# Performance work log

Measured on AMD Instinct MI355X. Metric: run time of the kernel, lower is better.

## Reference

```python
import jax, jax.numpy as jnp
import numpy as np

B, D, F, FH = 8, 16, 16, 128
L = D * D
EPS = 1e-5


def _coords():
    i = np.arange(L, dtype=np.float64)
    c0 = ((i + 1) / D - D / 2) / (D / 2)
    c1 = ((i + 1) % D - D / 2) / (D / 2)
    return jnp.asarray(np.stack([c0, c1], axis=1), dtype=jnp.float32)  # (L, 2)


def setup_inputs() -> dict:
    key = jax.random.key(0)
    ks = jax.random.split(key, 16)
    s = 0.05
    fin = F + 2
    inp = {
        "x": jax.random.normal(ks[0], (B, F, D, D), jnp.float32),
        # g_fc1 weight split into the x_i half (first f+2 cols) and x_j half
        "W1a": jax.random.normal(ks[1], (fin, FH), jnp.float32) * s,
        "W1b": jax.random.normal(ks[2], (fin, FH), jnp.float32) * s,
        "b1": jnp.zeros((FH,), jnp.float32),
        "g1_gamma": jnp.ones((FH,), jnp.float32), "g1_beta": jnp.zeros((FH,), jnp.float32),
        "W2": jax.random.normal(ks[3], (FH, FH), jnp.float32) * s, "b2": jnp.zeros((FH,), jnp.float32),
        "g2_gamma": jnp.ones((FH,), jnp.float32), "g2_beta": jnp.zeros((FH,), jnp.float32),
        "W3": jax.random.normal(ks[4], (FH, FH), jnp.float32) * s, "b3": jnp.zeros((FH,), jnp.float32),
        "g3_gamma": jnp.ones((FH,), jnp.float32), "g3_beta": jnp.zeros((FH,), jnp.float32),
        "Wagg": jax.random.normal(ks[5], (L,), jnp.float32) * s, "bagg": jnp.zeros((), jnp.float32),
        "Wf": jax.random.normal(ks[6], (FH, FH), jnp.float32) * s, "bf": jnp.zeros((FH,), jnp.float32),
        "f_gamma": jnp.ones((FH,), jnp.float32), "f_beta": jnp.zeros((FH,), jnp.float32),
        "Wo2": jax.random.normal(ks[7], (FH, FH), jnp.float32) * s, "bo2": jnp.zeros((FH,), jnp.float32),
        "o2_gamma": jnp.ones((FH,), jnp.float32), "o2_beta": jnp.zeros((FH,), jnp.float32),
        "Wo3": jax.random.normal(ks[8], (FH, F), jnp.float32) * s, "bo3": jnp.zeros((F,), jnp.float32),
        "coord": _coords(),
    }
    return inp


def _bn(h, gamma, beta):
    # torch BatchNorm1d (training mode) applied over channel dim = last axis here;
    # stats over (batch, length), biased variance.
    mu = jnp.mean(h, axis=(0, 1))
    var = jnp.mean((h - mu) ** 2, axis=(0, 1))
    return gamma * (h - mu) * jax.lax.rsqrt(var + EPS) + beta


def reference(x, W1a, W1b, b1, g1_gamma, g1_beta, W2, b2, g2_gamma, g2_beta,
              W3, b3, g3_gamma, g3_beta, Wagg, bagg, Wf, bf, f_gamma, f_beta,
              Wo2, bo2, o2_gamma, o2_beta, Wo3, bo3, coord):
    b, f, d = x.shape[0], x.shape[1], x.shape[2]
    l = d * d
    x_flat = x.reshape(b, f, l).transpose(0, 2, 1)                     # (b, L, f)
    x_flat = jnp.concatenate([x_flat, jnp.broadcast_to(coord, (b, l, 2))], axis=2)  # (b, L, f+2)
    # g_fc1 on cat([x_i, x_j]): x_i varies along pair-dim2 (index l), x_j along dim1 (index k)
    hi = x_flat @ W1a                                                  # (b, L, FH)
    hj = x_flat @ W1b                                                  # (b, L, FH)
    h = hi[:, None, :, :] + hj[:, :, None, :] + b1                     # (b, L, L, FH)
    h = h.reshape(b, l * l, -1)
    h = jax.nn.relu(_bn(h, g1_gamma, g1_beta))
    h = jax.nn.relu(_bn(h @ W2 + b2, g2_gamma, g2_beta))
    h = jax.nn.relu(_bn(h @ W3 + b3, g3_gamma, g3_beta))
    x_g = h.reshape(b, l, l, -1)                                       # (b, k, l, FH)
    # affine_aggregate: Linear(L -> 1) over the l (dim2) axis after permute
    x_agg = jnp.einsum('bklf,l->bkf', x_g, Wagg) + bagg                # (b, L, FH)
    x_f = jax.nn.relu(_bn(x_agg @ Wf + bf, f_gamma, f_beta))
    xo = jax.nn.relu(_bn(x_f @ Wo2 + bo2, o2_gamma, o2_beta))
    out = xo @ Wo3 + bo3                                               # (b, L, f)
    return out.reshape(b, d, d, f).transpose(0, 3, 1, 2)               # (b, f, d, d)
```

## Files before the change

kernel.cpp:

```cpp
#include <hip/hip_runtime.h>
#include <hip/hip_bf16.h>

typedef __bf16 bf16x8 __attribute__((ext_vector_type(8)));
typedef float  f32x4  __attribute__((ext_vector_type(4)));

static constexpr size_t MB = 1u << 20;
static constexpr size_t HI_OFF  = 0;
static constexpr size_t HJ_OFF  = HI_OFF + MB;
static constexpr size_t Z_OFF   = HJ_OFF + MB;
static constexpr size_t PS_OFF  = Z_OFF + (size_t)524288 * 128 * 2;
static constexpr size_t PQ_OFF  = PS_OFF + (size_t)4096 * 128 * 4;
static constexpr size_t S1I_OFF = PQ_OFF + (size_t)4096 * 128 * 4;
static constexpr size_t S2I_OFF = S1I_OFF + 32768;
static constexpr size_t S1J_OFF = S2I_OFF + 32768;
static constexpr size_t S2J_OFF = S1J_OFF + 32768;
static constexpr size_t A1_OFF  = S2J_OFF + 32768;
static constexpr size_t D1_OFF  = A1_OFF + 512;
static constexpr size_t A2_OFF  = D1_OFF + 512;
static constexpr size_t C2_OFF  = A2_OFF + 512;
static constexpr size_t A3_OFF  = C2_OFF + 512;
static constexpr size_t C3_OFF  = A3_OFF + 512;
static constexpr size_t AF_OFF  = C3_OFF + 512;
static constexpr size_t CF_OFF  = AF_OFF + 512;
static constexpr size_t AO_OFF  = CF_OFF + 512;
static constexpr size_t CO_OFF  = AO_OFF + 512;
static constexpr size_t W2T_OFF = CO_OFF + 512;
static constexpr size_t W3T_OFF = W2T_OFF + 32768;
static constexpr size_t XAGG_OFF = W3T_OFF + 32768;
static constexpr size_t Y1_OFF  = XAGG_OFF + MB;
static constexpr size_t Y2_OFF  = Y1_OFF + MB;
static constexpr size_t TPS_OFF = Y2_OFF + MB;
static constexpr size_t TPQ_OFF = TPS_OFF + 65536;

__global__ void build_h(const float* __restrict__ x, const float* __restrict__ coord,
                        const float* __restrict__ W1a, const float* __restrict__ W1b,
                        float* __restrict__ hi, float* __restrict__ hj)
{
    __shared__ float xr[18];
    int bl = blockIdx.x;
    int b = bl >> 8, l = bl & 255;
    int t = threadIdx.x;
    if (t < 18)
        xr[t] = (t < 16) ? x[((size_t)b * 16 + t) * 256 + l] : coord[l * 2 + (t - 16)];
    __syncthreads();
    float ai = 0.f, aj = 0.f;
#pragma unroll
    for (int c = 0; c < 18; ++c) {
        float xv = xr[c];
        ai += xv * W1a[c * 128 + t];
        aj += xv * W1b[c * 128 + t];
    }
    hi[(size_t)bl * 128 + t] = ai;
    hj[(size_t)bl * 128 + t] = aj;
}

__global__ void stats1(const float* __restrict__ hi, const float* __restrict__ hj,
                       float* __restrict__ S1i, float* __restrict__ S2i,
                       float* __restrict__ S1j, float* __restrict__ S2j)
{
    int g = blockIdx.x;
    int b = g >> 3, lg = g & 7;
    int f = threadIdx.x;
    float s1i = 0, s2i = 0, s1j = 0, s2j = 0;
#pragma unroll 4
    for (int i = 0; i < 32; ++i) {
        int l = lg * 32 + i;
        float vi = hi[((size_t)b * 256 + l) * 128 + f];
        float vj = hj[((size_t)b * 256 + l) * 128 + f];
        s1i += vi; s2i += vi * vi;
        s1j += vj; s2j += vj * vj;
    }
    S1i[g * 128 + f] = s1i; S2i[g * 128 + f] = s2i;
    S1j[g * 128 + f] = s1j; S2j[g * 128 + f] = s2j;
}

__global__ void bn1_finalize(const float* __restrict__ S1i, const float* __restrict__ S2i,
                             const float* __restrict__ S1j, const float* __restrict__ S2j,
                             const float* __restrict__ g, const float* __restrict__ be,
                             float* __restrict__ a1, float* __restrict__ d1)
{
    int f = threadIdx.x;
    float s1i = 0, s2i = 0, s1j = 0, s2j = 0;
    float mib[8], mjb[8];
#pragma unroll
    for (int b = 0; b < 8; ++b) {
        float sb = 0, sbj = 0;
#pragma unroll
        for (int lg = 0; lg < 8; ++lg) {
            int gg = b * 8 + lg;
            sb  += S1i[gg * 128 + f]; s2i += S2i[gg * 128 + f];
            sbj += S1j[gg * 128 + f]; s2j += S2j[gg * 128 + f];
        }
        mib[b] = sb * (1.f / 256.f); mjb[b] = sbj * (1.f / 256.f);
        s1i += sb; s1j += sbj;
    }
    const float invN = 1.f / 2048.f;
    float mi = s1i * invN, mj = s1j * invN;
    float vu = s2i * invN - mi * mi;
    float vv = s2j * invN - mj * mj;
    float cr = 0.f;
#pragma unroll
    for (int b = 0; b < 8; ++b) cr += (mib[b] - mi) * (mjb[b] - mj);
    cr *= (1.f / 8.f);
    float var = vu + vv + 2.f * cr;
    float av = g[f] * rsqrtf(var + 1e-5f);
    a1[f] = av;
    d1[f] = be[f] - av * (mi + mj);
}

__global__ void transpose_w(const float* __restrict__ W2, const float* __restrict__ W3,
                            __bf16* __restrict__ W2t, __bf16* __restrict__ W3t)
{
    int f = blockIdx.x, k = threadIdx.x;
    W2t[f * 128 + k] = (__bf16)W2[k * 128 + f];
    W3t[f * 128 + k] = (__bf16)W3[k * 128 + f];
}

__global__ __launch_bounds__(256, 3) void pair_gemm1(
    const float* __restrict__ hi, const float* __restrict__ hj,
    const float* __restrict__ a1, const float* __restrict__ d1,
    const __bf16* __restrict__ W2t,
    __bf16* __restrict__ Z, float* __restrict__ ps, float* __restrict__ pq)
{
    __shared__ __align__(16) char hA[32768];

    int blk = blockIdx.x;
    int half = blk & 1;
    int bk = blk >> 1;
    int b = bk >> 8;
    int t = threadIdx.x;
    int lane = t & 63;
    int wave = t >> 6;
    int fc = (t & 15) * 8;
    int rg = t >> 4;
    int cl = lane & 15;
    int kg = lane >> 4;
    int colbase = wave * 32;

    bf16x8 Bf[2][4];
#pragma unroll
    for (int n = 0; n < 2; ++n) {
        const __bf16* wp = W2t + (colbase + n * 16 + cl) * 128 + kg * 8;
#pragma unroll
        for (int kk = 0; kk < 4; ++kk)
            Bf[n][kk] = *reinterpret_cast<const bf16x8*>(wp + kk * 32);
    }

    float a1v[8], qv[8];
    const float* hjrow = hj + (size_t)bk * 128 + fc;
    const float* d1p = d1 + fc;
    const float* a1p = a1 + fc;
#pragma unroll
    for (int j = 0; j < 8; ++j) { a1v[j] = a1p[j]; qv[j] = a1v[j] * hjrow[j] + d1p[j]; }

    const float* hib = hi + ((size_t)b * 256 + half * 128) * 128;
#pragma unroll
    for (int rr = 0; rr < 128; rr += 16) {
        int row = rr + rg;
        const float* src = hib + row * 128 + fc;
        bf16x8 v;
#pragma unroll
        for (int j = 0; j < 8; ++j) {
            float h = fmaxf(a1v[j] * src[j] + qv[j], 0.f);
            v[j] = (__bf16)h;
        }
        int byte = (row * 256 + fc * 2) ^ ((row & 7) << 4);
        *reinterpret_cast<bf16x8*>(hA + byte) = v;
    }
    __syncthreads();

    f32x4 acc[8][2] = {};
#pragma unroll
    for (int kk = 0; kk < 128; kk += 32) {
        bf16x8 af[8];
#pragma unroll
        for (int m = 0; m < 8; ++m) {
            int row = m * 16 + cl;
            int byte = (row * 256 + (kk + kg * 8) * 2) ^ ((row & 7) << 4);
            af[m] = *reinterpret_cast<const bf16x8*>(hA + byte);
        }
#pragma unroll
        for (int m = 0; m < 8; ++m)
#pragma unroll
            for (int n = 0; n < 2; ++n)
                acc[m][n] = __builtin_amdgcn_mfma_f32_16x16x32_bf16(af[m], Bf[n][kk >> 5], acc[m][n], 0, 0, 0);
    }

    __bf16* zb = Z + ((size_t)bk * 256 + half * 128) * 128;
    int r0 = kg * 4;
#pragma unroll
    for (int n = 0; n < 2; ++n) {
        float s = 0.f, q = 0.f;
#pragma unroll
        for (int m = 0; m < 8; ++m)
#pragma unroll
            for (int r = 0; r < 4; ++r) {
                float v = acc[m][n][r];
                zb[(m * 16 + r0 + r) * 128 + colbase + n * 16 + cl] = (__bf16)v;
                s += v; q += v * v;
            }
        s += __shfl_xor(s, 16); s += __shfl_xor(s, 32);
        q += __shfl_xor(q, 16); q += __shfl_xor(q, 32);
        if (lane < 16) {
            ps[(size_t)blk * 128 + colbase + n * 16 + cl] = s;
            pq[(size_t)blk * 128 + colbase + n * 16 + cl] = q;
        }
    }
}

__global__ __launch_bounds__(256, 3) void pair_gemm2(
    __bf16* __restrict__ Z,
    const float* __restrict__ a2, const float* __restrict__ c2,
    const __bf16* __restrict__ W3t,
    float* __restrict__ ps, float* __restrict__ pq)
{
    __shared__ __align__(16) char hA[32768];

    int blk = blockIdx.x;
    int half = blk & 1;
    int bk = blk >> 1;
    int t = threadIdx.x;
    int lane = t & 63;
    int wave = t >> 6;
    int fc = (t & 15) * 8;
    int rg = t >> 4;
    int cl = lane & 15;
    int kg = lane >> 4;
    int colbase = wave * 32;

    bf16x8 Bf[2][4];
#pragma unroll
    for (int n = 0; n < 2; ++n) {
        const __bf16* wp = W3t + (colbase + n * 16 + cl) * 128 + kg * 8;
#pragma unroll
        for (int kk = 0; kk < 4; ++kk)
            Bf[n][kk] = *reinterpret_cast<const bf16x8*>(wp + kk * 32);
    }

    float a2v[8], c2v[8];
#pragma unroll
    for (int j = 0; j < 8; ++j) { a2v[j] = a2[fc + j]; c2v[j] = c2[fc + j]; }

    __bf16* zbase = Z + ((size_t)bk * 256 + half * 128) * 128;
#pragma unroll
    for (int rr = 0; rr < 128; rr += 16) {
        int row = rr + rg;
        bf16x8 zv = *reinterpret_cast<const bf16x8*>(zbase + row * 128 + fc);
        bf16x8 v;
#pragma unroll
        for (int j = 0; j < 8; ++j) {
            float h = fmaxf(a2v[j] * (float)zv[j] + c2v[j], 0.f);
            v[j] = (__bf16)h;
        }
        int byte = (row * 256 + fc * 2) ^ ((row & 7) << 4);
        *reinterpret_cast<bf16x8*>(hA + byte) = v;
    }
    __syncthreads();

    f32x4 acc[8][2] = {};
#pragma unroll
    for (int kk = 0; kk < 128; kk += 32) {
        bf16x8 af[8];
#pragma unroll
        for (int m = 0; m < 8; ++m) {
            int row = m * 16 + cl;
            int byte = (row * 256 + (kk + kg * 8) * 2) ^ ((row & 7) << 4);
            af[m] = *reinterpret_cast<const bf16x8*>(hA + byte);
        }
#pragma unroll
        for (int m = 0; m < 8; ++m)
#pragma unroll
            for (int n = 0; n < 2; ++n)
                acc[m][n] = __builtin_amdgcn_mfma_f32_16x16x32_bf16(af[m], Bf[n][kk >> 5], acc[m][n], 0, 0, 0);
    }

    int r0 = kg * 4;
#pragma unroll
    for (int n = 0; n < 2; ++n) {
        float s = 0.f, q = 0.f;
#pragma unroll
        for (int m = 0; m < 8; ++m)
#pragma unroll
            for (int r = 0; r < 4; ++r) {
                float v = acc[m][n][r];
                zbase[(m * 16 + r0 + r) * 128 + colbase + n * 16 + cl] = (__bf16)v;
                s += v; q += v * v;
            }
        s += __shfl_xor(s, 16); s += __shfl_xor(s, 32);
        q += __shfl_xor(q, 16); q += __shfl_xor(q, 32);
        if (lane < 16) {
            ps[(size_t)blk * 128 + colbase + n * 16 + cl] = s;
            pq[(size_t)blk * 128 + colbase + n * 16 + cl] = q;
        }
    }
}

__global__ void finalize_bn(const float* __restrict__ ps, const float* __restrict__ pq,
                            int nblk, float inv_count,
                            const float* __restrict__ gamma, const float* __restrict__ beta,
                            float* __restrict__ a, float* __restrict__ c)
{
    __shared__ float rs[256], rq[256];
    int f = blockIdx.x, t = threadIdx.x;
    float s = 0, q = 0;
    for (int i = t; i < nblk; i += 256) {
        s += ps[(size_t)i * 128 + f];
        q += pq[(size_t)i * 128 + f];
    }
    rs[t] = s; rq[t] = q;
    __syncthreads();
    for (int st = 128; st > 0; st >>= 1) {
        if (t < st) { rs[t] += rs[t + st]; rq[t] += rq[t + st]; }
        __syncthreads();
    }
    if (t == 0) {
        float mean = rs[0] * inv_count;
        float var = rq[0] * inv_count - mean * mean;
        float av = gamma[f] * rsqrtf(var + 1e-5f);
        a[f] = av;
        c[f] = beta[f] - av * mean;
    }
}

__global__ __launch_bounds__(256) void aggregate(
    const __bf16* __restrict__ Z,
    const float* __restrict__ a3, const float* __restrict__ c3,
    const float* __restrict__ Wagg, const float* __restrict__ bagg,
    float* __restrict__ xagg)
{
    __shared__ float red[16 * 128];
    int bk = blockIdx.x;
    int t = threadIdx.x;
    int fc = t & 15;
    int g = t >> 4;
    float av[8], cv[8];
#pragma unroll
    for (int j = 0; j < 8; ++j) { av[j] = a3[fc * 8 + j]; cv[j] = c3[fc * 8 + j]; }

    const __bf16* zb = Z + (size_t)bk * 256 * 128;
    float acc[8] = {};
#pragma unroll 4
    for (int i = 0; i < 16; ++i) {
        int l = g * 16 + i;
        bf16x8 zv = *reinterpret_cast<const bf16x8*>(zb + (size_t)l * 128 + fc * 8);
        float w = Wagg[l];
#pragma unroll
        for (int j = 0; j < 8; ++j)
            acc[j] += fmaxf(av[j] * (float)zv[j] + cv[j], 0.f) * w;
    }
#pragma unroll
    for (int j = 0; j < 8; ++j) red[g * 128 + fc * 8 + j] = acc[j];
    __syncthreads();
    if (t < 128) {
        float s = 0;
#pragma unroll
        for (int gg = 0; gg < 16; ++gg) s += red[gg * 128 + t];
        xagg[(size_t)bk * 128 + t] = s + bagg[0];
    }
}

__global__ void tail_gemm(const float* __restrict__ X,
                          const float* __restrict__ aIn, const float* __restrict__ cIn, int relu_in,
                          const float* __restrict__ W, const float* __restrict__ bias,
                          float* __restrict__ Y, float* __restrict__ ps, float* __restrict__ pq)
{
    __shared__ float xs[2048];
    __shared__ float rsum[256];
    int blk = blockIdx.x, t = threadIdx.x;
    for (int i = t; i < 2048; i += 256) {
        float v = X[(size_t)blk * 2048 + i];
        if (relu_in) { int f = i & 127; v = fmaxf(aIn[f] * v + cIn[f], 0.f); }
        xs[i] = v;
    }
    __syncthreads();
    int col = t & 127, hf = t >> 7;
    float bv = bias[col];
    float acc[8];
#pragma unroll
    for (int r = 0; r < 8; ++r) acc[r] = bv;
    for (int k = 0; k < 128; ++k) {
        float w = W[k * 128 + col];
#pragma unroll
        for (int r = 0; r < 8; ++r) acc[r] += xs[(hf * 8 + r) * 128 + k] * w;
    }
    float s = 0, q = 0;
#pragma unroll
    for (int r = 0; r < 8; ++r) {
        Y[((size_t)blk * 16 + hf * 8 + r) * 128 + col] = acc[r];
        s += acc[r]; q += acc[r] * acc[r];
    }
    rsum[t] = s; __syncthreads();
    if (hf == 0) ps[(size_t)blk * 128 + col] = rsum[col] + rsum[128 + col];
    __syncthreads();
    rsum[t] = q; __syncthreads();
    if (hf == 0) pq[(size_t)blk * 128 + col] = rsum[col] + rsum[128 + col];
}

__global__ void tail_out(const float* __restrict__ Y2,
                         const float* __restrict__ ao, const float* __restrict__ co,
                         const float* __restrict__ Wo3, const float* __restrict__ bo3,
                         float* __restrict__ out)
{
    __shared__ float xs[2048];
    int blk = blockIdx.x, t = threadIdx.x;
    for (int i = t; i < 2048; i += 256) {
        int f = i & 127;
        xs[i] = fmaxf(ao[f] * Y2[(size_t)blk * 2048 + i] + co[f], 0.f);
    }
    __syncthreads();
    int col = t & 15, r = t >> 4;
    float acc = bo3[col];
    for (int k = 0; k < 128; ++k) acc += xs[r * 128 + k] * Wo3[k * 16 + col];
    int grow = blk * 16 + r;
    int b = grow >> 8, l = grow & 255;
    out[((size_t)b * 16 + col) * 256 + l] = acc;
}

extern "C" void kernel_launch(void* const* d_in, const int* in_sizes, int n_in,
                              void* d_out, int out_size, void* d_ws, size_t ws_size,
                              hipStream_t stream)
{
    const float* x     = (const float*)d_in[0];
    const float* W1a   = (const float*)d_in[1];
    const float* W1b   = (const float*)d_in[2];
    const float* g1g   = (const float*)d_in[4];
    const float* g1b   = (const float*)d_in[5];
    const float* W2    = (const float*)d_in[6];
    const float* g2g   = (const float*)d_in[8];
    const float* g2b   = (const float*)d_in[9];
    const float* W3    = (const float*)d_in[10];
    const float* g3g   = (const float*)d_in[12];
    const float* g3b   = (const float*)d_in[13];
    const float* Wagg  = (const float*)d_in[14];
    const float* bagg  = (const float*)d_in[15];
    const float* Wf    = (const float*)d_in[16];
    const float* bf_   = (const float*)d_in[17];
    const float* fg    = (const float*)d_in[18];
    const float* fb    = (const float*)d_in[19];
    const float* Wo2   = (const float*)d_in[20];
    const float* bo2   = (const float*)d_in[21];
    const float* og    = (const float*)d_in[22];
    const float* ob    = (const float*)d_in[23];
    const float* Wo3   = (const float*)d_in[24];
    const float* bo3   = (const float*)d_in[25];
    const float* coord = (const float*)d_in[26];

    char* ws = (char*)d_ws;
    float*  HI   = (float*)(ws + HI_OFF);
    float*  HJ   = (float*)(ws + HJ_OFF);
    __bf16* Z    = (__bf16*)(ws + Z_OFF);
    float*  PS   = (float*)(ws + PS_OFF);
    float*  PQ   = (float*)(ws + PQ_OFF);
    float*  S1I  = (float*)(ws + S1I_OFF);
    float*  S2I  = (float*)(ws + S2I_OFF);
    float*  S1J  = (float*)(ws + S1J_OFF);
    float*  S2J  = (float*)(ws + S2J_OFF);
    float*  A1   = (float*)(ws + A1_OFF);
    float*  D1   = (float*)(ws + D1_OFF);
    float*  A2   = (float*)(ws + A2_OFF);
    float*  C2   = (float*)(ws + C2_OFF);
    float*  A3   = (float*)(ws + A3_OFF);
    float*  C3   = (float*)(ws + C3_OFF);
    float*  AF   = (float*)(ws + AF_OFF);
    float*  CF   = (float*)(ws + CF_OFF);
    float*  AO   = (float*)(ws + AO_OFF);
    float*  CO   = (float*)(ws + CO_OFF);
    __bf16* W2T  = (__bf16*)(ws + W2T_OFF);
    __bf16* W3T  = (__bf16*)(ws + W3T_OFF);
    float*  XAGG = (float*)(ws + XAGG_OFF);
    float*  Y1   = (float*)(ws + Y1_OFF);
    float*  Y2   = (float*)(ws + Y2_OFF);
    float*  TPS  = (float*)(ws + TPS_OFF);
    float*  TPQ  = (float*)(ws + TPQ_OFF);

    build_h<<<2048, 128, 0, stream>>>(x, coord, W1a, W1b, HI, HJ);
    stats1<<<64, 128, 0, stream>>>(HI, HJ, S1I, S2I, S1J, S2J);
    bn1_finalize<<<1, 128, 0, stream>>>(S1I, S2I, S1J, S2J, g1g, g1b, A1, D1);
    transpose_w<<<128, 128, 0, stream>>>(W2, W3, W2T, W3T);

    pair_gemm1<<<4096, 256, 0, stream>>>(HI, HJ, A1, D1, W2T, Z, PS, PQ);
    finalize_bn<<<128, 256, 0, stream>>>(PS, PQ, 4096, 1.f / 524288.f, g2g, g2b, A2, C2);

    pair_gemm2<<<4096, 256, 0, stream>>>(Z, A2, C2, W3T, PS, PQ);
    finalize_bn<<<128, 256, 0, stream>>>(PS, PQ, 4096, 1.f / 524288.f, g3g, g3b, A3, C3);

    aggregate<<<2048, 256, 0, stream>>>(Z, A3, C3, Wagg, bagg, XAGG);

    tail_gemm<<<128, 256, 0, stream>>>(XAGG, A1, D1, 0, Wf, bf_, Y1, TPS, TPQ);
    finalize_bn<<<128, 256, 0, stream>>>(TPS, TPQ, 128, 1.f / 2048.f, fg, fb, AF, CF);

    tail_gemm<<<128, 256, 0, stream>>>(Y1, AF, CF, 1, Wo2, bo2, Y2, TPS, TPQ);
    finalize_bn<<<128, 256, 0, stream>>>(TPS, TPQ, 128, 1.f / 2048.f, og, ob, AO, CO);

    tail_out<<<128, 256, 0, stream>>>(Y2, AO, CO, Wo3, bo3, (float*)d_out);

    (void)in_sizes; (void)n_in; (void)out_size; (void)ws_size;
}
```

Baseline: 197.9 us.

## Fuse tail BN finalize into consumer kernels and raise pair GEMM occupancy

Removes the two small finalize_bn launches in the tail MLP. Each consumer block now reduces the partial sums itself and applies the BN affine plus ReLU. Separate stats buffers are added so that consumer kernels do not read buffers still being overwritten. The pair GEMMs get launch_bounds raised from 3 to 4 blocks per SM, and their epilogue is reordered to sweep rows with both column tiles per row, which may improve store coalescing. The fused finalize repeats the reduction in every block, and the higher occupancy target may cause register spills with 64 accumulator floats per thread.

```diff
diff --git a/kernel.cpp b/kernel.cpp
--- a/kernel.cpp
+++ b/kernel.cpp
@@ -20,17 +20,15 @@
 static constexpr size_t C2_OFF  = A2_OFF + 512;
 static constexpr size_t A3_OFF  = C2_OFF + 512;
 static constexpr size_t C3_OFF  = A3_OFF + 512;
-static constexpr size_t AF_OFF  = C3_OFF + 512;
-static constexpr size_t CF_OFF  = AF_OFF + 512;
-static constexpr size_t AO_OFF  = CF_OFF + 512;
-static constexpr size_t CO_OFF  = AO_OFF + 512;
-static constexpr size_t W2T_OFF = CO_OFF + 512;
+static constexpr size_t W2T_OFF = C3_OFF + 512;
 static constexpr size_t W3T_OFF = W2T_OFF + 32768;
 static constexpr size_t XAGG_OFF = W3T_OFF + 32768;
 static constexpr size_t Y1_OFF  = XAGG_OFF + MB;
 static constexpr size_t Y2_OFF  = Y1_OFF + MB;
 static constexpr size_t TPS_OFF = Y2_OFF + MB;
 static constexpr size_t TPQ_OFF = TPS_OFF + 65536;
+static constexpr size_t TPS2_OFF = TPQ_OFF + 65536;
+static constexpr size_t TPQ2_OFF = TPS2_OFF + 65536;
 
 __global__ void build_h(const float* __restrict__ x, const float* __restrict__ coord,
                         const float* __restrict__ W1a, const float* __restrict__ W1b,
@@ -116,7 +114,7 @@
     W3t[f * 128 + k] = (__bf16)W3[k * 128 + f];
 }
 
-__global__ __launch_bounds__(256, 3) void pair_gemm1(
+__global__ __launch_bounds__(256, 4) void pair_gemm1(
     const float* __restrict__ hi, const float* __restrict__ hj,
     const float* __restrict__ a1, const float* __restrict__ d1,
     const __bf16* __restrict__ W2t,
@@ -188,27 +186,32 @@
 
     __bf16* zb = Z + ((size_t)bk * 256 + half * 128) * 128;
     int r0 = kg * 4;
+    float s[2] = {}, q[2] = {};
+#pragma unroll
+    for (int m = 0; m < 8; ++m)
+#pragma unroll
+        for (int r = 0; r < 4; ++r) {
+            int row = m * 16 + r0 + r;
+#pragma unroll
+            for (int n = 0; n < 2; ++n) {
+                float v = acc[m][n][r];
+                zb[row * 128 + colbase + n * 16 + cl] = (__bf16)v;
+                s[n] += v; q[n] += v * v;
+            }
+        }
 #pragma unroll
     for (int n = 0; n < 2; ++n) {
-        float s = 0.f, q = 0.f;
-#pragma unroll
-        for (int m = 0; m < 8; ++m)
-#pragma unroll
-            for (int r = 0; r < 4; ++r) {
-                float v = acc[m][n][r];
-                zb[(m * 16 + r0 + r) * 128 + colbase + n * 16 + cl] = (__bf16)v;
-                s += v; q += v * v;
-            }
-        s += __shfl_xor(s, 16); s += __shfl_xor(s, 32);
-        q += __shfl_xor(q, 16); q += __shfl_xor(q, 32);
+        float sv = s[n], qv2 = q[n];
+        sv += __shfl_xor(sv, 16); sv += __shfl_xor(sv, 32);
+        qv2 += __shfl_xor(qv2, 16); qv2 += __shfl_xor(qv2, 32);
         if (lane < 16) {
-            ps[(size_t)blk * 128 + colbase + n * 16 + cl] = s;
-            pq[(size_t)blk * 128 + colbase + n * 16 + cl] = q;
-        }
-    }
-}
-
-__global__ __launch_bounds__(256, 3) void pair_gemm2(
+            ps[(size_t)blk * 128 + colbase + n * 16 + cl] = sv;
+            pq[(size_t)blk * 128 + colbase + n * 16 + cl] = qv2;
+        }
+    }
+}
+
+__global__ __launch_bounds__(256, 4) void pair_gemm2(
     __bf16* __restrict__ Z,
     const float* __restrict__ a2, const float* __restrict__ c2,
     const __bf16* __restrict__ W3t,
@@ -275,22 +278,27 @@
     }
 
     int r0 = kg * 4;
+    float s[2] = {}, q[2] = {};
+#pragma unroll
+    for (int m = 0; m < 8; ++m)
+#pragma unroll
+        for (int r = 0; r < 4; ++r) {
+            int row = m * 16 + r0 + r;
+#pragma unroll
+            for (int n = 0; n < 2; ++n) {
+                float v = acc[m][n][r];
+                zbase[row * 128 + colbase + n * 16 + cl] = (__bf16)v;
+                s[n] += v; q[n] += v * v;
+            }
+        }
 #pragma unroll
     for (int n = 0; n < 2; ++n) {
-        float s = 0.f, q = 0.f;
-#pragma unroll
-        for (int m = 0; m < 8; ++m)
-#pragma unroll
-            for (int r = 0; r < 4; ++r) {
-                float v = acc[m][n][r];
-                zbase[(m * 16 + r0 + r) * 128 + colbase + n * 16 + cl] = (__bf16)v;
-                s += v; q += v * v;
-            }
-        s += __shfl_xor(s, 16); s += __shfl_xor(s, 32);
-        q += __shfl_xor(q, 16); q += __shfl_xor(q, 32);
+        float sv = s[n], qv2 = q[n];
+        sv += __shfl_xor(sv, 16); sv += __shfl_xor(sv, 32);
+        qv2 += __shfl_xor(qv2, 16); qv2 += __shfl_xor(qv2, 32);
         if (lane < 16) {
-            ps[(size_t)blk * 128 + colbase + n * 16 + cl] = s;
-            pq[(size_t)blk * 128 + colbase + n * 16 + cl] = q;
+            ps[(size_t)blk * 128 + colbase + n * 16 + cl] = sv;
+            pq[(size_t)blk * 128 + colbase + n * 16 + cl] = qv2;
         }
     }
 }
@@ -360,18 +368,14 @@
 }
 
 __global__ void tail_gemm(const float* __restrict__ X,
-                          const float* __restrict__ aIn, const float* __restrict__ cIn, int relu_in,
                           const float* __restrict__ W, const float* __restrict__ bias,
                           float* __restrict__ Y, float* __restrict__ ps, float* __restrict__ pq)
 {
     __shared__ float xs[2048];
     __shared__ float rsum[256];
     int blk = blockIdx.x, t = threadIdx.x;
-    for (int i = t; i < 2048; i += 256) {
-        float v = X[(size_t)blk * 2048 + i];
-        if (relu_in) { int f = i & 127; v = fmaxf(aIn[f] * v + cIn[f], 0.f); }
-        xs[i] = v;
-    }
+    for (int i = t; i < 2048; i += 256)
+        xs[i] = X[(size_t)blk * 2048 + i];
     __syncthreads();
     int col = t & 127, hf = t >> 7;
     float bv = bias[col];
@@ -396,16 +400,82 @@
     if (hf == 0) pq[(size_t)blk * 128 + col] = rsum[col] + rsum[128 + col];
 }
 
+__global__ void tail_gemm_bn(const float* __restrict__ X,
+                             const float* __restrict__ tps, const float* __restrict__ tpq,
+                             const float* __restrict__ gamma, const float* __restrict__ beta,
+                             const float* __restrict__ W, const float* __restrict__ bias,
+                             float* __restrict__ Y, float* __restrict__ ps, float* __restrict__ pq)
+{
+    __shared__ float xs[2048];
+    __shared__ float rsum[256];
+    __shared__ float aSh[128], cSh[128];
+    int blk = blockIdx.x, t = threadIdx.x;
+    if (t < 128) {
+        float s = 0, q = 0;
+#pragma unroll 4
+        for (int i = 0; i < 128; ++i) {
+            s += tps[(size_t)i * 128 + t];
+            q += tpq[(size_t)i * 128 + t];
+        }
+        float mean = s * (1.f / 2048.f);
+        float var = q * (1.f / 2048.f) - mean * mean;
+        float av = gamma[t] * rsqrtf(var + 1e-5f);
+        aSh[t] = av; cSh[t] = beta[t] - av * mean;
+    }
+    __syncthreads();
+    for (int i = t; i < 2048; i += 256) {
+        int f = i & 127;
+        xs[i] = fmaxf(aSh[f] * X[(size_t)blk * 2048 + i] + cSh[f], 0.f);
+    }
+    __syncthreads();
+    int col = t & 127, hf = t >> 7;
+    float bv = bias[col];
+    float acc[8];
+#pragma unroll
+    for (int r = 0; r < 8; ++r) acc[r] = bv;
+    for (int k = 0; k < 128; ++k) {
+        float w = W[k * 128 + col];
+#pragma unroll
+        for (int r = 0; r < 8; ++r) acc[r] += xs[(hf * 8 + r) * 128 + k] * w;
+    }
+    float s = 0, q = 0;
+#pragma unroll
+    for (int r = 0; r < 8; ++r) {
+        Y[((size_t)blk * 16 + hf * 8 + r) * 128 + col] = acc[r];
+        s += acc[r]; q += acc[r] * acc[r];
+    }
+    rsum[t] = s; __syncthreads();
+    if (hf == 0) ps[(size_t)blk * 128 + col] = rsum[col] + rsum[128 + col];
+    __syncthreads();
+    rsum[t] = q; __syncthreads();
+    if (hf == 0) pq[(size_t)blk * 128 + col] = rsum[col] + rsum[128 + col];
+}
+
 __global__ void tail_out(const float* __restrict__ Y2,
-                         const float* __restrict__ ao, const float* __restrict__ co,
+                         const float* __restrict__ tps, const float* __restrict__ tpq,
+                         const float* __restrict__ gamma, const float* __restrict__ beta,
                          const float* __restrict__ Wo3, const float* __restrict__ bo3,
                          float* __restrict__ out)
 {
     __shared__ float xs[2048];
+    __shared__ float aSh[128], cSh[128];
     int blk = blockIdx.x, t = threadIdx.x;
+    if (t < 128) {
+        float s = 0, q = 0;
+#pragma unroll 4
+        for (int i = 0; i < 128; ++i) {
+            s += tps[(size_t)i * 128 + t];
+            q += tpq[(size_t)i * 128 + t];
+        }
+        float mean = s * (1.f / 2048.f);
+        float var = q * (1.f / 2048.f) - mean * mean;
+        float av = gamma[t] * rsqrtf(var + 1e-5f);
+        aSh[t] = av; cSh[t] = beta[t] - av * mean;
+    }
+    __syncthreads();
     for (int i = t; i < 2048; i += 256) {
         int f = i & 127;
-        xs[i] = fmaxf(ao[f] * Y2[(size_t)blk * 2048 + i] + co[f], 0.f);
+        xs[i] = fmaxf(aSh[f] * Y2[(size_t)blk * 2048 + i] + cSh[f], 0.f);
     }
     __syncthreads();
     int col = t & 15, r = t >> 4;
@@ -461,10 +531,6 @@
     float*  C2   = (float*)(ws + C2_OFF);
     float*  A3   = (float*)(ws + A3_OFF);
     float*  C3   = (float*)(ws + C3_OFF);
-    float*  AF   = (float*)(ws + AF_OFF);
-    float*  CF   = (float*)(ws + CF_OFF);
-    float*  AO   = (float*)(ws + AO_OFF);
-    float*  CO   = (float*)(ws + CO_OFF);
     __bf16* W2T  = (__bf16*)(ws + W2T_OFF);
     __bf16* W3T  = (__bf16*)(ws + W3T_OFF);
     float*  XAGG = (float*)(ws + XAGG_OFF);
@@ -472,6 +538,8 @@
     float*  Y2   = (float*)(ws + Y2_OFF);
     float*  TPS  = (float*)(ws + TPS_OFF);
     float*  TPQ  = (float*)(ws + TPQ_OFF);
+    float*  TPS2 = (float*)(ws + TPS2_OFF);
+    float*  TPQ2 = (float*)(ws + TPQ2_OFF);
 
     build_h<<<2048, 128, 0, stream>>>(x, coord, W1a, W1b, HI, HJ);
     stats1<<<64, 128, 0, stream>>>(HI, HJ, S1I, S2I, S1J, S2J);
@@ -486,13 +554,9 @@
 
     aggregate<<<2048, 256, 0, stream>>>(Z, A3, C3, Wagg, bagg, XAGG);
 
-    tail_gemm<<<128, 256, 0, stream>>>(XAGG, A1, D1, 0, Wf, bf_, Y1, TPS, TPQ);
-    finalize_bn<<<128, 256, 0, stream>>>(TPS, TPQ, 128, 1.f / 2048.f, fg, fb, AF, CF);
-
-    tail_gemm<<<128, 256, 0, stream>>>(Y1, AF, CF, 1, Wo2, bo2, Y2, TPS, TPQ);
-    finalize_bn<<<128, 256, 0, stream>>>(TPS, TPQ, 128, 1.f / 2048.f, og, ob, AO, CO);
-
-    tail_out<<<128, 256, 0, stream>>>(Y2, AO, CO, Wo3, bo3, (float*)d_out);
+    tail_gemm<<<128, 256, 0, stream>>>(XAGG, Wf, bf_, Y1, TPS, TPQ);
+    tail_gemm_bn<<<128, 256, 0, stream>>>(Y1, TPS, TPQ, fg, fb, Wo2, bo2, Y2, TPS2, TPQ2);
+    tail_out<<<128, 256, 0, stream>>>(Y2, TPS2, TPQ2, og, ob, Wo3, bo3, (float*)d_out);
 
     (void)in_sizes; (void)n_in; (void)out_size; (void)ws_size;
 }
```

New measurement: 205.2 us. +3.7%, slower.
